# Optimization experiments

Measured on AMD Instinct MI355X. Metric: run time of the kernel, lower is better.

## Reference

```python
import jax, jax.numpy as jnp
import numpy as np

B, N = 128, 65536
POS_FRAC = 0.02  # sparse positives, realistic for detection


def setup_inputs() -> dict:
    key = jax.random.key(0)
    k1, k2 = jax.random.split(key)
    pred = jax.random.normal(k1, (B, N), dtype=jnp.float32)
    label = (jax.random.uniform(k2, (B, N)) < POS_FRAC).astype(jnp.float32)
    return {"pred": pred, "label": label}


def _focal_loss_with_mask(pred, label, gamma=2.0, alpha=0.75, negative_ratio=3.0):
    # BCE with logits, elementwise: y*softplus(-x) + (1-y)*softplus(x)
    loss = label * jax.nn.softplus(-pred) + (1.0 - label) * jax.nn.softplus(pred)
    p = jax.nn.sigmoid(pred)
    p_t = label * p + (1.0 - label) * (1.0 - p)
    loss = loss * (1.0 - p_t) ** gamma
    loss = loss * (label * alpha + (1.0 - label) * (1.0 - alpha))

    fn_mask = (p < 0.5) & (label == 1.0)
    fp_mask = (p >= 0.5) & (label == 0.0)

    # --- hard negative mining (vectorized rank-based selection) ---
    pos_mask = label > 0
    num_pos = pos_mask.sum(axis=1, keepdims=True)              # [B,1]
    num_neg = jnp.floor(negative_ratio * num_pos).astype(jnp.int32)  # int() truncation as in torch
    loss_m = jnp.where(pos_mask, -jnp.inf, loss)               # positives sorted last
    order = jnp.argsort(-loss_m, axis=1)                       # descending sort indices
    ranks = jnp.argsort(order, axis=1)                         # rank of each element
    neg_mask = ranks < num_neg
    relevant = pos_mask | neg_mask

    w = alpha / (1.0 - alpha)
    loss = jnp.where(fn_mask | fp_mask, loss * w, loss)
    rm = relevant.astype(loss.dtype)
    return (loss * rm).sum() / rm.sum()


def reference(pred, label):
    return _focal_loss_with_mask(pred, label)
```

## Files before the change

### kernel.cpp

```cpp
#include <hip/hip_runtime.h>
#include <cstdint>
#include <cstddef>

constexpr int B_ROWS = 128;
constexpr int N_COLS = 65536;
constexpr int CAP    = 4096;

constexpr size_t OFF_SLABCNT = 0;
constexpr size_t OFF_SLABNP  = (size_t)8 << 20;
constexpr size_t OFF_SLABSP  = ((size_t)8 << 20) + 4096;
constexpr size_t OFF_CAND    = (size_t)9 << 20;
constexpr size_t OFF_MISC    = (size_t)12 << 20;
constexpr size_t MO_NUMPOS   = 0;
constexpr size_t MO_SPOS     = 512;
constexpr size_t MO_CANDBIN  = 1024;
constexpr size_t MO_R1       = 1536;
constexpr size_t MO_KARR     = 2048;
constexpr size_t MO_CANDCNT  = 2560;
constexpr size_t MO_SABOVE   = 3072;
constexpr size_t MO_AUTO64   = 3584;
constexpr size_t MO_GNUM     = 4608;
constexpr size_t MO_GDEN     = 4616;
constexpr size_t MO_GDONE    = 4620;
constexpr size_t OFF_KEYS    = (size_t)16 << 20;

__device__ __forceinline__ unsigned key_from_pred(float x) {
  unsigned b = __float_as_uint(x);
  return (b & 0x80000000u) ? ~b : (b | 0x80000000u);
}
__device__ __forceinline__ float pred_from_key(unsigned k) {
  unsigned b = (k & 0x80000000u) ? (k ^ 0x80000000u) : ~k;
  return __uint_as_float(b);
}

__device__ __forceinline__ float neg_loss(float x) {
  float ax = fabsf(x);
  float e  = expf(-ax);
  float p  = (x >= 0.0f) ? 1.0f / (1.0f + e) : e / (1.0f + e);
  float sp = fmaxf(x, 0.0f) + log1pf(e);
  float f  = p;
  float l  = sp * f * f * 0.25f;
  return (p >= 0.5f) ? l * 3.0f : l;
}
__device__ __forceinline__ float pos_loss(float x) {
  float ax = fabsf(x);
  float e  = expf(-ax);
  float p  = (x >= 0.0f) ? 1.0f / (1.0f + e) : e / (1.0f + e);
  float sp = fmaxf(-x, 0.0f) + log1pf(e);
  float f  = 1.0f - p;
  float l  = sp * f * f * 0.75f;
  return (p < 0.5f) ? l * 3.0f : l;
}
__device__ __forceinline__ float loss_from_key(unsigned k) { return neg_loss(pred_from_key(k)); }

__device__ void suffix_scan(int* c, float* l, int M) {
  const int T = blockDim.x;
  const int i0 = threadIdx.x, i1 = threadIdx.x + T;
  for (int d = 1; d < M; d <<= 1) {
    int vi0 = 0, vi1 = 0; float vf0 = 0.0f, vf1 = 0.0f;
    const bool h0 = i0 < M, h1 = i1 < M;
    if (h0) { vi0 = c[i0] + ((i0 + d < M) ? c[i0 + d] : 0);
              vf0 = l[i0] + ((i0 + d < M) ? l[i0 + d] : 0.0f); }
    if (h1) { vi1 = c[i1] + ((i1 + d < M) ? c[i1 + d] : 0);
              vf1 = l[i1] + ((i1 + d < M) ? l[i1 + d] : 0.0f); }
    __syncthreads();
    if (h0) { c[i0] = vi0; l[i0] = vf0; }
    if (h1) { c[i1] = vi1; l[i1] = vf1; }
    __syncthreads();
  }
}
__device__ void suffix_scan_i(int* c, int M) {
  const int T = blockDim.x;
  const int i0 = threadIdx.x, i1 = threadIdx.x + T;
  for (int d = 1; d < M; d <<= 1) {
    int v0 = 0, v1 = 0;
    const bool h0 = i0 < M, h1 = i1 < M;
    if (h0) v0 = c[i0] + ((i0 + d < M) ? c[i0 + d] : 0);
    if (h1) v1 = c[i1] + ((i1 + d < M) ? c[i1 + d] : 0);
    __syncthreads();
    if (h0) c[i0] = v0;
    if (h1) c[i1] = v1;
    __syncthreads();
  }
}
__device__ int find_cut(const int* sc, int M, int r, int* ctrl) {
  __syncthreads();
  if (threadIdx.x == 0) *ctrl = -1;
  __syncthreads();
  int loc = -1;
  for (int i = threadIdx.x; i < M; i += blockDim.x)
    if (sc[i] >= r) loc = i;
  if (loc >= 0) atomicMax(ctrl, loc);
  __syncthreads();
  return *ctrl;
}

constexpr int K1_TPB = 256;
constexpr int K1_SEGS = 8;
constexpr int K1_SEG_ELEMS = N_COLS / K1_SEGS;
constexpr int K1_ITERS = K1_SEG_ELEMS / (K1_TPB * 4);

template <bool STORE_KEYS>
__global__ __launch_bounds__(K1_TPB)
void k1_hist(const float* __restrict__ pred, const float* __restrict__ label,
             int* __restrict__ slabCnt, int* __restrict__ slabNP, float* __restrict__ slabSP,
             unsigned* __restrict__ keys)
{
  __shared__ int   hcnt[2048];
  __shared__ int   wnp[K1_TPB / 64];
  __shared__ float wsp[K1_TPB / 64];
  const int tid = threadIdx.x;
  for (int i = tid; i < 2048; i += K1_TPB) hcnt[i] = 0;
  __syncthreads();

  const int blk = blockIdx.x;
  const size_t base = (size_t)blk * K1_SEG_ELEMS;
  const float4* p4 = reinterpret_cast<const float4*>(pred + base);
  const float4* l4 = reinterpret_cast<const float4*>(label + base);
  uint4* k4 = STORE_KEYS ? reinterpret_cast<uint4*>(keys + base) : nullptr;

  int npos = 0; float spos = 0.0f;
  for (int it = 0; it < K1_ITERS; ++it) {
    const int vi = it * K1_TPB + tid;
    const float4 pv = p4[vi];
    const float4 lv = l4[vi];
    const float xs[4] = {pv.x, pv.y, pv.z, pv.w};
    const float ys[4] = {lv.x, lv.y, lv.z, lv.w};
    unsigned ks[4];
#pragma unroll
    for (int j = 0; j < 4; ++j) {
      const float x = xs[j];
      if (ys[j] > 0.5f) {
        npos += 1;
        spos += pos_loss(x);
        ks[j] = 0u;
      } else {
        const unsigned key = key_from_pred(x);
        ks[j] = key;
        atomicAdd(&hcnt[key >> 21], 1);
      }
    }
    if (STORE_KEYS) { uint4 uk; uk.x = ks[0]; uk.y = ks[1]; uk.z = ks[2]; uk.w = ks[3]; k4[vi] = uk; }
  }

#pragma unroll
  for (int off = 32; off > 0; off >>= 1) {
    npos += __shfl_down(npos, off);
    spos += __shfl_down(spos, off);
  }
  const int wid = tid >> 6, lane = tid & 63;
  if (lane == 0) { wnp[wid] = npos; wsp[wid] = spos; }
  __syncthreads();
  if (tid == 0) {
    int tn = 0; float ts = 0.0f;
    for (int i = 0; i < K1_TPB / 64; ++i) { tn += wnp[i]; ts += wsp[i]; }
    slabNP[blk] = tn;
    slabSP[blk] = ts;
  }
  for (int i = tid; i < 2048; i += K1_TPB)
    slabCnt[(size_t)blk * 2048 + i] = hcnt[i];
}

__global__ __launch_bounds__(1024)
void k2a_cut(const int* __restrict__ slabCnt, const int* __restrict__ slabNP,
             const float* __restrict__ slabSP,
             int* __restrict__ numPos, float* __restrict__ SPos,
             int* __restrict__ candBin, unsigned long long* __restrict__ auto64,
             int* __restrict__ r1Arr, int* __restrict__ kArr,
             int* __restrict__ candCnt, float* __restrict__ S_above,
             double* __restrict__ gNum, int* __restrict__ gDen, int* __restrict__ gDone)
{
  __shared__ int s_cnt[2048];
  __shared__ int s_ctrl;
  __shared__ int s_np;
  __shared__ float s_sp;
  const int tid = threadIdx.x, row = blockIdx.x;

  if (tid == 0) {
    int tn = 0; float ts = 0.0f;
    for (int s = 0; s < K1_SEGS; ++s) { tn += slabNP[row * K1_SEGS + s]; ts += slabSP[row * K1_SEGS + s]; }
    s_np = tn; s_sp = ts;
  }
  for (int i = tid; i < 2048; i += 1024) {
    int v = 0;
#pragma unroll
    for (int s = 0; s < K1_SEGS; ++s) v += slabCnt[((size_t)(row * K1_SEGS + s)) * 2048 + i];
    s_cnt[i] = v;
  }
  __syncthreads();

  const int np = s_np;
  const int nneg = N_COLS - np;
  const int k = (3 * np < nneg) ? 3 * np : nneg;

  suffix_scan_i(s_cnt, 2048);
  int b1 = -1;
  if (k > 0) b1 = find_cut(s_cnt, 2048, k, &s_ctrl);

  if (tid == 0) {
    numPos[row]  = np;
    SPos[row]    = s_sp;
    candCnt[row] = 0;
    S_above[row] = 0.0f;
    kArr[row]    = k;
    if (k > 0) {
      const int above = (b1 + 1 < 2048) ? s_cnt[b1 + 1] : 0;
      candBin[row] = b1;
      auto64[row]  = (unsigned long long)(b1 + 1) << 21;
      r1Arr[row]   = k - above;
    } else {
      candBin[row] = -1;
      auto64[row]  = 1ull << 32;
      r1Arr[row]   = 0;
    }
  }
  if (row == 0 && tid == 1) { *gNum = 0.0; *gDen = 0; *gDone = 0; }
}

constexpr int K2B_TPB = 256;
constexpr int K2B_SEGS = 16;
constexpr int K2B_SEG_ELEMS = N_COLS / K2B_SEGS;
constexpr int K2B_ITERS = K2B_SEG_ELEMS / (K2B_TPB * 4);

template <bool USE_KEYS>
__global__ __launch_bounds__(K2B_TPB)
void k2b_stream(const float* __restrict__ pred, const float* __restrict__ label,
                const unsigned* __restrict__ keys,
                const int* __restrict__ candBin, const unsigned long long* __restrict__ auto64,
                unsigned* __restrict__ candList, int* __restrict__ candCnt,
                float* __restrict__ S_above)
{
  __shared__ unsigned s_cand[K2B_SEG_ELEMS];
  __shared__ int      s_cnt;
  __shared__ int      s_base;
  __shared__ float    wacc[K2B_TPB / 64];

  const int tid = threadIdx.x;
  const int row = blockIdx.x / K2B_SEGS;
  const int seg = blockIdx.x % K2B_SEGS;
  const size_t base = (size_t)row * N_COLS + (size_t)seg * K2B_SEG_ELEMS;
  const int cb = candBin[row];
  const unsigned long long at = auto64[row];
  const int lane = tid & 63, wid = tid >> 6;

  if (tid == 0) s_cnt = 0;
  __syncthreads();

  float acc = 0.0f;
  for (int it = 0; it < K2B_ITERS; ++it) {
    unsigned ks[4];
    if (USE_KEYS) {
      const uint4 kv = reinterpret_cast<const uint4*>(keys + base)[it * K2B_TPB + tid];
      ks[0] = kv.x; ks[1] = kv.y; ks[2] = kv.z; ks[3] = kv.w;
    } else {
      const float4 pv = reinterpret_cast<const float4*>(pred + base)[it * K2B_TPB + tid];
      const float4 lv = reinterpret_cast<const float4*>(label + base)[it * K2B_TPB + tid];
      const float xs[4] = {pv.x, pv.y, pv.z, pv.w};
      const float ys[4] = {lv.x, lv.y, lv.z, lv.w};
#pragma unroll
      for (int j = 0; j < 4; ++j) ks[j] = (ys[j] > 0.5f) ? 0u : key_from_pred(xs[j]);
    }
#pragma unroll
    for (int j = 0; j < 4; ++j) {
      const unsigned key = ks[j];
      if (key == 0u) continue;
      if ((unsigned long long)key >= at) {
        acc += loss_from_key(key);
      } else if ((int)(key >> 21) == cb) {
        const int idx = atomicAdd(&s_cnt, 1);
        s_cand[idx] = key;
      }
    }
  }

#pragma unroll
  for (int off = 32; off > 0; off >>= 1) acc += __shfl_down(acc, off);
  if (lane == 0) wacc[wid] = acc;
  __syncthreads();
  if (tid == 0) {
    float t = 0.0f;
    for (int i = 0; i < K2B_TPB / 64; ++i) t += wacc[i];
    unsafeAtomicAdd(&S_above[row], t);
    s_base = atomicAdd(&candCnt[row], s_cnt);
  }
  __syncthreads();

  const int cnt = s_cnt, gbase = s_base;
  for (int i = tid; i < cnt; i += K2B_TPB) {
    const int g = gbase + i;
    if (g < CAP) candList[(size_t)row * CAP + g] = s_cand[i];
  }
}

template <bool USE_KEYS>
__device__ void stream_bin(const float* __restrict__ pred, const float* __restrict__ label,
                           const unsigned* __restrict__ keys, int row, int b1, int b2,
                           int* hcnt, float* hloss)
{
  const size_t base = (size_t)row * N_COLS;
  const int tid = threadIdx.x;
  for (int it = 0; it < N_COLS / (1024 * 4); ++it) {
    unsigned ks[4];
    if (USE_KEYS) {
      const uint4 kv = reinterpret_cast<const uint4*>(keys + base)[it * 1024 + tid];
      ks[0] = kv.x; ks[1] = kv.y; ks[2] = kv.z; ks[3] = kv.w;
    } else {
      const float4 pv = reinterpret_cast<const float4*>(pred + base)[it * 1024 + tid];
      const float4 lv = reinterpret_cast<const float4*>(label + base)[it * 1024 + tid];
      const float xs[4] = {pv.x, pv.y, pv.z, pv.w};
      const float ys[4] = {lv.x, lv.y, lv.z, lv.w};
#pragma unroll
      for (int j = 0; j < 4; ++j) ks[j] = (ys[j] > 0.5f) ? 0u : key_from_pred(xs[j]);
    }
#pragma unroll
    for (int j = 0; j < 4; ++j) {
      const unsigned key = ks[j];
      if (!key) continue;
      if ((int)(key >> 21) != b1) continue;
      if (b2 < 0) {
        const int b = (key >> 10) & 0x7FF;
        atomicAdd(&hcnt[b], 1);
        atomicAdd(&hloss[b], loss_from_key(key));
      } else {
        if ((int)((key >> 10) & 0x7FF) != b2) continue;
        const int b = key & 0x3FF;
        atomicAdd(&hcnt[b], 1);
        atomicAdd(&hloss[b], loss_from_key(key));
      }
    }
  }
}

template <bool USE_KEYS>
__global__ __launch_bounds__(1024)
void k2c_refine(const float* __restrict__ pred, const float* __restrict__ label,
                const unsigned* __restrict__ keys,
                const int* __restrict__ numPos, const float* __restrict__ SPos,
                const int* __restrict__ candBin, const int* __restrict__ r1Arr,
                const int* __restrict__ kArr, const int* __restrict__ candCnt,
                const unsigned* __restrict__ candList, const float* __restrict__ S_above,
                double* __restrict__ gNum, int* __restrict__ gDen, int* __restrict__ gDone,
                float* __restrict__ out)
{
  __shared__ unsigned s_key[CAP];
  __shared__ float    s_lv[CAP];
  __shared__ int      h_cnt[2048];
  __shared__ float    h_loss[2048];
  __shared__ int      r3cnt[1024];
  __shared__ float    r3loss[1024];
  __shared__ int      s_ctrl;

  const int tid = threadIdx.x, row = blockIdx.x;
  const int np = numPos[row];
  const int k  = kArr[row];
  float S = 0.0f;

  if (k > 0) {
    const int r1 = r1Arr[row];
    const int b1 = candBin[row];
    const int cc = candCnt[row];

    for (int i = tid; i < 2048; i += 1024) { h_cnt[i] = 0; h_loss[i] = 0.0f; }
    __syncthreads();

    int b2, r2;
    if (cc <= CAP) {
      for (int i = tid; i < cc; i += 1024) {
        const unsigned key = candList[(size_t)row * CAP + i];
        const float l = loss_from_key(key);
        s_key[i] = key; s_lv[i] = l;
        const int b = (key >> 10) & 0x7FF;
        atomicAdd(&h_cnt[b], 1);
        atomicAdd(&h_loss[b], l);
      }
      __syncthreads();
      suffix_scan(h_cnt, h_loss, 2048);
      b2 = find_cut(h_cnt, 2048, r1, &s_ctrl);
      r2 = r1 - ((b2 + 1 < 2048) ? h_cnt[b2 + 1] : 0);
      S += (b2 + 1 < 2048) ? h_loss[b2 + 1] : 0.0f;
      __syncthreads();

      for (int i = tid; i < 1024; i += 1024) { r3cnt[i] = 0; r3loss[i] = 0.0f; }
      __syncthreads();
      for (int i = tid; i < cc; i += 1024) {
        const unsigned key = s_key[i];
        if ((int)((key >> 10) & 0x7FF) == b2) {
          atomicAdd(&r3cnt[key & 0x3FF], 1);
          atomicAdd(&r3loss[key & 0x3FF], s_lv[i]);
        }
      }
      __syncthreads();
    } else {
      stream_bin<USE_KEYS>(pred, label, keys, row, b1, -1, h_cnt, h_loss);
      __syncthreads();
      suffix_scan(h_cnt, h_loss, 2048);
      b2 = find_cut(h_cnt, 2048, r1, &s_ctrl);
      r2 = r1 - ((b2 + 1 < 2048) ? h_cnt[b2 + 1] : 0);
      S += (b2 + 1 < 2048) ? h_loss[b2 + 1] : 0.0f;
      __syncthreads();
      for (int i = tid; i < 1024; i += 1024) { r3cnt[i] = 0; r3loss[i] = 0.0f; }
      __syncthreads();
      stream_bin<USE_KEYS>(pred, label, keys, row, b1, b2, r3cnt, r3loss);
      __syncthreads();
    }

    for (int i = tid; i < 1024; i += 1024) { h_cnt[i] = r3cnt[i]; h_loss[i] = r3loss[i]; }
    __syncthreads();
    suffix_scan(h_cnt, h_loss, 1024);
    const int b3 = find_cut(h_cnt, 1024, r2, &s_ctrl);
    const int r3 = r2 - ((b3 + 1 < 1024) ? h_cnt[b3 + 1] : 0);
    S += (b3 + 1 < 1024) ? h_loss[b3 + 1] : 0.0f;
    S += (float)r3 * (r3loss[b3] / (float)r3cnt[b3]);
  }

  if (tid == 0) {
    const double contrib = (double)SPos[row] +
                           (k > 0 ? (double)S + (double)S_above[row] : 0.0);
    const int dcontrib = np + (k > 0 ? k : 0);
    unsafeAtomicAdd(gNum, contrib);
    atomicAdd(gDen, dcontrib);
    __threadfence();
    const int old = atomicAdd(gDone, 1);
    if (old == B_ROWS - 1) {
      const double num = unsafeAtomicAdd(gNum, 0.0);
      const int    den = atomicAdd(gDen, 0);
      out[0] = (float)(num / (double)den);
    }
  }
}

extern "C" void kernel_launch(void* const* d_in, const int* in_sizes, int n_in,
                              void* d_out, int out_size, void* d_ws, size_t ws_size,
                              hipStream_t stream)
{
  const float* pred  = (const float*)d_in[0];
  const float* label = (const float*)d_in[1];
  float* out = (float*)d_out;
  char* ws = (char*)d_ws;

  int*      slabCnt = (int*)(ws + OFF_SLABCNT);
  int*      slabNP  = (int*)(ws + OFF_SLABNP);
  float*    slabSP  = (float*)(ws + OFF_SLABSP);
  unsigned* cand    = (unsigned*)(ws + OFF_CAND);
  char*     misc    = ws + OFF_MISC;
  int*      numPos  = (int*)(misc + MO_NUMPOS);
  float*    SPos    = (float*)(misc + MO_SPOS);
  int*      candBin = (int*)(misc + MO_CANDBIN);
  int*      r1Arr   = (int*)(misc + MO_R1);
  int*      kArr    = (int*)(misc + MO_KARR);
  int*      candCnt = (int*)(misc + MO_CANDCNT);
  float*    S_above = (float*)(misc + MO_SABOVE);
  unsigned long long* auto64 = (unsigned long long*)(misc + MO_AUTO64);
  double*   gNum    = (double*)(misc + MO_GNUM);
  int*      gDen    = (int*)(misc + MO_GDEN);
  int*      gDone   = (int*)(misc + MO_GDONE);
  unsigned* keys    = (unsigned*)(ws + OFF_KEYS);

  const bool useKeys = ws_size >= OFF_KEYS + (size_t)B_ROWS * N_COLS * sizeof(unsigned);

  const dim3 g1(B_ROWS * K1_SEGS), t1(K1_TPB);
  const dim3 g2a(B_ROWS), t2a(1024);
  const dim3 g2b(B_ROWS * K2B_SEGS), t2b(K2B_TPB);
  const dim3 g2c(B_ROWS), t2c(1024);

  if (useKeys) {
    k1_hist<true><<<g1, t1, 0, stream>>>(pred, label, slabCnt, slabNP, slabSP, keys);
    k2a_cut<<<g2a, t2a, 0, stream>>>(slabCnt, slabNP, slabSP, numPos, SPos, candBin, auto64,
                                     r1Arr, kArr, candCnt, S_above, gNum, gDen, gDone);
    k2b_stream<true><<<g2b, t2b, 0, stream>>>(pred, label, keys, candBin, auto64, cand, candCnt, S_above);
    k2c_refine<true><<<g2c, t2c, 0, stream>>>(pred, label, keys, numPos, SPos, candBin, r1Arr, kArr,
                                              candCnt, cand, S_above, gNum, gDen, gDone, out);
  } else {
    k1_hist<false><<<g1, t1, 0, stream>>>(pred, label, slabCnt, slabNP, slabSP, nullptr);
    k2a_cut<<<g2a, t2a, 0, stream>>>(slabCnt, slabNP, slabSP, numPos, SPos, candBin, auto64,
                                     r1Arr, kArr, candCnt, S_above, gNum, gDen, gDone);
    k2b_stream<false><<<g2b, t2b, 0, stream>>>(pred, label, nullptr, candBin, auto64, cand, candCnt, S_above);
    k2c_refine<false><<<g2c, t2c, 0, stream>>>(pred, label, nullptr, numPos, SPos, candBin, r1Arr, kArr,
                                               candCnt, cand, S_above, gNum, gDen, gDone, out);
  }
}
```

Baseline: 175.9 us.

## Fuse four-kernel pipeline into one cooperative kernel with grid syncs

Replaces the four separate launches (histogram, cut, stream, refine) with a single cooperative kernel that uses grid.sync between phases. It also drops the precomputed keys buffer, so pred and label are re-read instead. The refine phase moves from 1024-thread blocks to 256-thread blocks with a two-level suffix scan. The aim is to cut launch overhead and inter-kernel gaps, at the cost of grid-wide barriers, fewer threads per row in the refine phase, and limited grid size (four blocks per CU assumed).

After: 603.3 us. 3.43x slower.

```diff
diff --git a/kernel.cpp b/kernel.cpp
--- a/kernel.cpp
+++ b/kernel.cpp
@@ -1,10 +1,19 @@
 #include <hip/hip_runtime.h>
+#include <hip/hip_cooperative_groups.h>
 #include <cstdint>
 #include <cstddef>
+
+namespace cg = cooperative_groups;
 
 constexpr int B_ROWS = 128;
 constexpr int N_COLS = 65536;
 constexpr int CAP    = 4096;
+constexpr int TPB    = 256;
+constexpr int VB1    = 1024;
+constexpr int SEGS   = VB1 / B_ROWS;
+constexpr int SEG_ELEMS = N_COLS / SEGS;
+constexpr int ITERS  = SEG_ELEMS / (TPB * 4);
+constexpr int CAND_SH = 4096;
 
 constexpr size_t OFF_SLABCNT = 0;
 constexpr size_t OFF_SLABNP  = (size_t)8 << 20;
@@ -21,8 +30,6 @@
 constexpr size_t MO_AUTO64   = 3584;
 constexpr size_t MO_GNUM     = 4608;
 constexpr size_t MO_GDEN     = 4616;
-constexpr size_t MO_GDONE    = 4620;
-constexpr size_t OFF_KEYS    = (size_t)16 << 20;
 
 __device__ __forceinline__ unsigned key_from_pred(float x) {
   unsigned b = __float_as_uint(x);
@@ -53,36 +60,29 @@
 }
 __device__ __forceinline__ float loss_from_key(unsigned k) { return neg_loss(pred_from_key(k)); }
 
-__device__ void suffix_scan(int* c, float* l, int M) {
-  const int T = blockDim.x;
-  const int i0 = threadIdx.x, i1 = threadIdx.x + T;
-  for (int d = 1; d < M; d <<= 1) {
-    int vi0 = 0, vi1 = 0; float vf0 = 0.0f, vf1 = 0.0f;
-    const bool h0 = i0 < M, h1 = i1 < M;
-    if (h0) { vi0 = c[i0] + ((i0 + d < M) ? c[i0 + d] : 0);
-              vf0 = l[i0] + ((i0 + d < M) ? l[i0 + d] : 0.0f); }
-    if (h1) { vi1 = c[i1] + ((i1 + d < M) ? c[i1 + d] : 0);
-              vf1 = l[i1] + ((i1 + d < M) ? l[i1 + d] : 0.0f); }
-    __syncthreads();
-    if (h0) { c[i0] = vi0; l[i0] = vf0; }
-    if (h1) { c[i1] = vi1; l[i1] = vf1; }
-    __syncthreads();
-  }
-}
-__device__ void suffix_scan_i(int* c, int M) {
-  const int T = blockDim.x;
-  const int i0 = threadIdx.x, i1 = threadIdx.x + T;
-  for (int d = 1; d < M; d <<= 1) {
-    int v0 = 0, v1 = 0;
-    const bool h0 = i0 < M, h1 = i1 < M;
-    if (h0) v0 = c[i0] + ((i0 + d < M) ? c[i0 + d] : 0);
-    if (h1) v1 = c[i1] + ((i1 + d < M) ? c[i1 + d] : 0);
-    __syncthreads();
-    if (h0) c[i0] = v0;
-    if (h1) c[i1] = v1;
-    __syncthreads();
-  }
-}
+__device__ void suffix_scan_2l(int* c, float* l, int M, int* tmpc, float* tmpl) {
+  const int t = threadIdx.x;
+  const int CH = M / TPB;
+  int cs = 0; float ls = 0.0f;
+  for (int j = 0; j < CH; ++j) { cs += c[t * CH + j]; ls += l[t * CH + j]; }
+  tmpc[t] = cs; tmpl[t] = ls;
+  __syncthreads();
+  for (int d = 1; d < TPB; d <<= 1) {
+    int v = tmpc[t] + ((t + d < TPB) ? tmpc[t + d] : 0);
+    float w = tmpl[t] + ((t + d < TPB) ? tmpl[t + d] : 0.0f);
+    __syncthreads();
+    tmpc[t] = v; tmpl[t] = w;
+    __syncthreads();
+  }
+  int runc = (t + 1 < TPB) ? tmpc[t + 1] : 0;
+  float runl = (t + 1 < TPB) ? tmpl[t + 1] : 0.0f;
+  for (int j = CH - 1; j >= 0; --j) {
+    runc += c[t * CH + j]; runl += l[t * CH + j];
+    c[t * CH + j] = runc;  l[t * CH + j] = runl;
+  }
+  __syncthreads();
+}
+
 __device__ int find_cut(const int* sc, int M, int r, int* ctrl) {
   __syncthreads();
   if (threadIdx.x == 0) *ctrl = -1;
@@ -95,337 +95,237 @@
   return *ctrl;
 }
 
-constexpr int K1_TPB = 256;
-constexpr int K1_SEGS = 8;
-constexpr int K1_SEG_ELEMS = N_COLS / K1_SEGS;
-constexpr int K1_ITERS = K1_SEG_ELEMS / (K1_TPB * 4);
-
-template <bool STORE_KEYS>
-__global__ __launch_bounds__(K1_TPB)
-void k1_hist(const float* __restrict__ pred, const float* __restrict__ label,
-             int* __restrict__ slabCnt, int* __restrict__ slabNP, float* __restrict__ slabSP,
-             unsigned* __restrict__ keys)
-{
-  __shared__ int   hcnt[2048];
-  __shared__ int   wnp[K1_TPB / 64];
-  __shared__ float wsp[K1_TPB / 64];
-  const int tid = threadIdx.x;
-  for (int i = tid; i < 2048; i += K1_TPB) hcnt[i] = 0;
-  __syncthreads();
-
-  const int blk = blockIdx.x;
-  const size_t base = (size_t)blk * K1_SEG_ELEMS;
+__device__ void stream_row_bin(const float* __restrict__ pred, const float* __restrict__ label,
+                               int row, int b1, int b2, int* hcnt, float* hloss) {
+  const size_t base = (size_t)row * N_COLS;
   const float4* p4 = reinterpret_cast<const float4*>(pred + base);
   const float4* l4 = reinterpret_cast<const float4*>(label + base);
-  uint4* k4 = STORE_KEYS ? reinterpret_cast<uint4*>(keys + base) : nullptr;
-
-  int npos = 0; float spos = 0.0f;
-  for (int it = 0; it < K1_ITERS; ++it) {
-    const int vi = it * K1_TPB + tid;
-    const float4 pv = p4[vi];
-    const float4 lv = l4[vi];
+  for (int it = 0; it < N_COLS / (TPB * 4); ++it) {
+    const float4 pv = p4[it * TPB + threadIdx.x];
+    const float4 lv = l4[it * TPB + threadIdx.x];
     const float xs[4] = {pv.x, pv.y, pv.z, pv.w};
     const float ys[4] = {lv.x, lv.y, lv.z, lv.w};
-    unsigned ks[4];
 #pragma unroll
     for (int j = 0; j < 4; ++j) {
-      const float x = xs[j];
-      if (ys[j] > 0.5f) {
-        npos += 1;
-        spos += pos_loss(x);
-        ks[j] = 0u;
+      if (ys[j] > 0.5f) continue;
+      const unsigned key = key_from_pred(xs[j]);
+      if ((int)(key >> 21) != b1) continue;
+      if (b2 < 0) {
+        atomicAdd(&hcnt[(key >> 10) & 0x7FF], 1);
+        atomicAdd(&hloss[(key >> 10) & 0x7FF], neg_loss(xs[j]));
       } else {
-        const unsigned key = key_from_pred(x);
-        ks[j] = key;
-        atomicAdd(&hcnt[key >> 21], 1);
-      }
-    }
-    if (STORE_KEYS) { uint4 uk; uk.x = ks[0]; uk.y = ks[1]; uk.z = ks[2]; uk.w = ks[3]; k4[vi] = uk; }
-  }
-
-#pragma unroll
-  for (int off = 32; off > 0; off >>= 1) {
-    npos += __shfl_down(npos, off);
-    spos += __shfl_down(spos, off);
-  }
-  const int wid = tid >> 6, lane = tid & 63;
-  if (lane == 0) { wnp[wid] = npos; wsp[wid] = spos; }
-  __syncthreads();
-  if (tid == 0) {
-    int tn = 0; float ts = 0.0f;
-    for (int i = 0; i < K1_TPB / 64; ++i) { tn += wnp[i]; ts += wsp[i]; }
-    slabNP[blk] = tn;
-    slabSP[blk] = ts;
-  }
-  for (int i = tid; i < 2048; i += K1_TPB)
-    slabCnt[(size_t)blk * 2048 + i] = hcnt[i];
-}
-
-__global__ __launch_bounds__(1024)
-void k2a_cut(const int* __restrict__ slabCnt, const int* __restrict__ slabNP,
-             const float* __restrict__ slabSP,
-             int* __restrict__ numPos, float* __restrict__ SPos,
-             int* __restrict__ candBin, unsigned long long* __restrict__ auto64,
-             int* __restrict__ r1Arr, int* __restrict__ kArr,
-             int* __restrict__ candCnt, float* __restrict__ S_above,
-             double* __restrict__ gNum, int* __restrict__ gDen, int* __restrict__ gDone)
+        if ((int)((key >> 10) & 0x7FF) != b2) continue;
+        atomicAdd(&hcnt[key & 0x3FF], 1);
+        atomicAdd(&hloss[key & 0x3FF], neg_loss(xs[j]));
+      }
+    }
+  }
+}
+
+__global__ __launch_bounds__(TPB, 4)
+void fused_all(const float* __restrict__ pred, const float* __restrict__ label,
+               int* __restrict__ slabCnt, int* __restrict__ slabNP, float* __restrict__ slabSP,
+               int* __restrict__ numPos, float* __restrict__ SPosArr,
+               int* __restrict__ candBin, unsigned long long* __restrict__ auto64,
+               int* __restrict__ r1Arr, int* __restrict__ kArr,
+               int* __restrict__ candCnt, float* __restrict__ S_above,
+               unsigned* __restrict__ candList,
+               double* __restrict__ gNum, int* __restrict__ gDen,
+               float* __restrict__ out)
 {
-  __shared__ int s_cnt[2048];
-  __shared__ int s_ctrl;
-  __shared__ int s_np;
-  __shared__ float s_sp;
-  const int tid = threadIdx.x, row = blockIdx.x;
-
-  if (tid == 0) {
-    int tn = 0; float ts = 0.0f;
-    for (int s = 0; s < K1_SEGS; ++s) { tn += slabNP[row * K1_SEGS + s]; ts += slabSP[row * K1_SEGS + s]; }
-    s_np = tn; s_sp = ts;
-  }
-  for (int i = tid; i < 2048; i += 1024) {
-    int v = 0;
-#pragma unroll
-    for (int s = 0; s < K1_SEGS; ++s) v += slabCnt[((size_t)(row * K1_SEGS + s)) * 2048 + i];
-    s_cnt[i] = v;
-  }
-  __syncthreads();
-
-  const int np = s_np;
-  const int nneg = N_COLS - np;
-  const int k = (3 * np < nneg) ? 3 * np : nneg;
-
-  suffix_scan_i(s_cnt, 2048);
-  int b1 = -1;
-  if (k > 0) b1 = find_cut(s_cnt, 2048, k, &s_ctrl);
-
-  if (tid == 0) {
-    numPos[row]  = np;
-    SPos[row]    = s_sp;
-    candCnt[row] = 0;
-    S_above[row] = 0.0f;
-    kArr[row]    = k;
-    if (k > 0) {
-      const int above = (b1 + 1 < 2048) ? s_cnt[b1 + 1] : 0;
-      candBin[row] = b1;
-      auto64[row]  = (unsigned long long)(b1 + 1) << 21;
-      r1Arr[row]   = k - above;
-    } else {
-      candBin[row] = -1;
-      auto64[row]  = 1ull << 32;
-      r1Arr[row]   = 0;
-    }
-  }
-  if (row == 0 && tid == 1) { *gNum = 0.0; *gDen = 0; *gDone = 0; }
-}
-
-constexpr int K2B_TPB = 256;
-constexpr int K2B_SEGS = 16;
-constexpr int K2B_SEG_ELEMS = N_COLS / K2B_SEGS;
-constexpr int K2B_ITERS = K2B_SEG_ELEMS / (K2B_TPB * 4);
-
-template <bool USE_KEYS>
-__global__ __launch_bounds__(K2B_TPB)
-void k2b_stream(const float* __restrict__ pred, const float* __restrict__ label,
-                const unsigned* __restrict__ keys,
-                const int* __restrict__ candBin, const unsigned long long* __restrict__ auto64,
-                unsigned* __restrict__ candList, int* __restrict__ candCnt,
-                float* __restrict__ S_above)
-{
-  __shared__ unsigned s_cand[K2B_SEG_ELEMS];
-  __shared__ int      s_cnt;
-  __shared__ int      s_base;
-  __shared__ float    wacc[K2B_TPB / 64];
+  cg::grid_group grid = cg::this_grid();
+  __shared__ __align__(16) char smem[26624];
+  int*      h_cnt  = (int*)smem;
+  float*    h_loss = (float*)(smem + 8192);
+  int*      r3c    = (int*)(smem + 16384);
+  float*    r3l    = (float*)(smem + 20480);
+  int*      tmpc   = (int*)(smem + 24576);
+  float*    tmpl   = (float*)(smem + 25600);
+  unsigned* candSh = (unsigned*)smem;
+  __shared__ int   s_ctrl, s_bcast, s_base;
+  __shared__ int   wnp[TPB / 64];
+  __shared__ float wsp[TPB / 64];
 
   const int tid = threadIdx.x;
-  const int row = blockIdx.x / K2B_SEGS;
-  const int seg = blockIdx.x % K2B_SEGS;
-  const size_t base = (size_t)row * N_COLS + (size_t)seg * K2B_SEG_ELEMS;
-  const int cb = candBin[row];
-  const unsigned long long at = auto64[row];
   const int lane = tid & 63, wid = tid >> 6;
 
-  if (tid == 0) s_cnt = 0;
-  __syncthreads();
-
-  float acc = 0.0f;
-  for (int it = 0; it < K2B_ITERS; ++it) {
-    unsigned ks[4];
-    if (USE_KEYS) {
-      const uint4 kv = reinterpret_cast<const uint4*>(keys + base)[it * K2B_TPB + tid];
-      ks[0] = kv.x; ks[1] = kv.y; ks[2] = kv.z; ks[3] = kv.w;
-    } else {
-      const float4 pv = reinterpret_cast<const float4*>(pred + base)[it * K2B_TPB + tid];
-      const float4 lv = reinterpret_cast<const float4*>(label + base)[it * K2B_TPB + tid];
+  for (int vb = blockIdx.x; vb < VB1; vb += gridDim.x) {
+    for (int i = tid; i < 2048; i += TPB) h_cnt[i] = 0;
+    __syncthreads();
+    const size_t base = (size_t)vb * SEG_ELEMS;
+    const float4* p4 = reinterpret_cast<const float4*>(pred + base);
+    const float4* l4 = reinterpret_cast<const float4*>(label + base);
+    int npos = 0; float spos = 0.0f;
+    for (int it = 0; it < ITERS; ++it) {
+      const float4 pv = p4[it * TPB + tid];
+      const float4 lv = l4[it * TPB + tid];
       const float xs[4] = {pv.x, pv.y, pv.z, pv.w};
       const float ys[4] = {lv.x, lv.y, lv.z, lv.w};
 #pragma unroll
-      for (int j = 0; j < 4; ++j) ks[j] = (ys[j] > 0.5f) ? 0u : key_from_pred(xs[j]);
-    }
-#pragma unroll
-    for (int j = 0; j < 4; ++j) {
-      const unsigned key = ks[j];
-      if (key == 0u) continue;
-      if ((unsigned long long)key >= at) {
-        acc += loss_from_key(key);
-      } else if ((int)(key >> 21) == cb) {
-        const int idx = atomicAdd(&s_cnt, 1);
-        s_cand[idx] = key;
-      }
-    }
-  }
-
-#pragma unroll
-  for (int off = 32; off > 0; off >>= 1) acc += __shfl_down(acc, off);
-  if (lane == 0) wacc[wid] = acc;
-  __syncthreads();
-  if (tid == 0) {
-    float t = 0.0f;
-    for (int i = 0; i < K2B_TPB / 64; ++i) t += wacc[i];
-    unsafeAtomicAdd(&S_above[row], t);
-    s_base = atomicAdd(&candCnt[row], s_cnt);
-  }
-  __syncthreads();
-
-  const int cnt = s_cnt, gbase = s_base;
-  for (int i = tid; i < cnt; i += K2B_TPB) {
-    const int g = gbase + i;
-    if (g < CAP) candList[(size_t)row * CAP + g] = s_cand[i];
-  }
-}
-
-template <bool USE_KEYS>
-__device__ void stream_bin(const float* __restrict__ pred, const float* __restrict__ label,
-                           const unsigned* __restrict__ keys, int row, int b1, int b2,
-                           int* hcnt, float* hloss)
-{
-  const size_t base = (size_t)row * N_COLS;
-  const int tid = threadIdx.x;
-  for (int it = 0; it < N_COLS / (1024 * 4); ++it) {
-    unsigned ks[4];
-    if (USE_KEYS) {
-      const uint4 kv = reinterpret_cast<const uint4*>(keys + base)[it * 1024 + tid];
-      ks[0] = kv.x; ks[1] = kv.y; ks[2] = kv.z; ks[3] = kv.w;
-    } else {
-      const float4 pv = reinterpret_cast<const float4*>(pred + base)[it * 1024 + tid];
-      const float4 lv = reinterpret_cast<const float4*>(label + base)[it * 1024 + tid];
+      for (int j = 0; j < 4; ++j) {
+        if (ys[j] > 0.5f) { npos += 1; spos += pos_loss(xs[j]); }
+        else atomicAdd(&h_cnt[key_from_pred(xs[j]) >> 21], 1);
+      }
+    }
+#pragma unroll
+    for (int off = 32; off > 0; off >>= 1) {
+      npos += __shfl_down(npos, off);
+      spos += __shfl_down(spos, off);
+    }
+    if (lane == 0) { wnp[wid] = npos; wsp[wid] = spos; }
+    __syncthreads();
+    if (tid == 0) {
+      int tn = 0; float ts = 0.0f;
+      for (int i = 0; i < TPB / 64; ++i) { tn += wnp[i]; ts += wsp[i]; }
+      slabNP[vb] = tn; slabSP[vb] = ts;
+    }
+    for (int i = tid; i < 2048; i += TPB) slabCnt[(size_t)vb * 2048 + i] = h_cnt[i];
+    __syncthreads();
+  }
+  grid.sync();
+
+  for (int row = blockIdx.x; row < B_ROWS; row += gridDim.x) {
+    for (int i = tid; i < 2048; i += TPB) {
+      int v = 0;
+#pragma unroll
+      for (int s = 0; s < SEGS; ++s) v += slabCnt[(size_t)(row * SEGS + s) * 2048 + i];
+      h_cnt[i] = v; h_loss[i] = 0.0f;
+    }
+    if (tid == 0) {
+      int tn = 0; float ts = 0.0f;
+      for (int s = 0; s < SEGS; ++s) { tn += slabNP[row * SEGS + s]; ts += slabSP[row * SEGS + s]; }
+      s_bcast = tn; wsp[0] = ts;
+    }
+    __syncthreads();
+    const int np = s_bcast;
+    const float sp = wsp[0];
+    const int nneg = N_COLS - np;
+    const int k = (3 * np < nneg) ? 3 * np : nneg;
+    suffix_scan_2l(h_cnt, h_loss, 2048, tmpc, tmpl);
+    int b1 = -1, r1 = 0; unsigned long long at = 1ull << 32;
+    if (k > 0) {
+      b1 = find_cut(h_cnt, 2048, k, &s_ctrl);
+      const int above = (b1 + 1 < 2048) ? h_cnt[b1 + 1] : 0;
+      r1 = k - above;
+      at = (unsigned long long)(b1 + 1) << 21;
+    }
+    if (tid == 0) {
+      numPos[row] = np; SPosArr[row] = sp;
+      candBin[row] = b1; auto64[row] = at; r1Arr[row] = r1; kArr[row] = k;
+      candCnt[row] = 0; S_above[row] = 0.0f;
+    }
+    __syncthreads();
+  }
+  if (blockIdx.x == 0 && tid == 0) { *gNum = 0.0; *gDen = 0; }
+  grid.sync();
+
+  for (int vb = blockIdx.x; vb < VB1; vb += gridDim.x) {
+    const int row = vb / SEGS;
+    const int cb = candBin[row];
+    const unsigned long long at = auto64[row];
+    if (tid == 0) s_bcast = 0;
+    __syncthreads();
+    const size_t base = (size_t)vb * SEG_ELEMS;
+    const float4* p4 = reinterpret_cast<const float4*>(pred + base);
+    const float4* l4 = reinterpret_cast<const float4*>(label + base);
+    float acc = 0.0f;
+    for (int it = 0; it < ITERS; ++it) {
+      const float4 pv = p4[it * TPB + tid];
+      const float4 lv = l4[it * TPB + tid];
       const float xs[4] = {pv.x, pv.y, pv.z, pv.w};
       const float ys[4] = {lv.x, lv.y, lv.z, lv.w};
 #pragma unroll
-      for (int j = 0; j < 4; ++j) ks[j] = (ys[j] > 0.5f) ? 0u : key_from_pred(xs[j]);
-    }
-#pragma unroll
-    for (int j = 0; j < 4; ++j) {
-      const unsigned key = ks[j];
-      if (!key) continue;
-      if ((int)(key >> 21) != b1) continue;
-      if (b2 < 0) {
-        const int b = (key >> 10) & 0x7FF;
-        atomicAdd(&hcnt[b], 1);
-        atomicAdd(&hloss[b], loss_from_key(key));
+      for (int j = 0; j < 4; ++j) {
+        if (ys[j] > 0.5f) continue;
+        const unsigned key = key_from_pred(xs[j]);
+        if ((unsigned long long)key >= at) {
+          acc += neg_loss(xs[j]);
+        } else if ((int)(key >> 21) == cb) {
+          const int idx = atomicAdd(&s_bcast, 1);
+          if (idx < CAND_SH) candSh[idx] = key;
+        }
+      }
+    }
+#pragma unroll
+    for (int off = 32; off > 0; off >>= 1) acc += __shfl_down(acc, off);
+    if (lane == 0) wsp[wid] = acc;
+    __syncthreads();
+    if (tid == 0) {
+      float t = 0.0f;
+      for (int i = 0; i < TPB / 64; ++i) t += wsp[i];
+      unsafeAtomicAdd(&S_above[row], t);
+      s_base = atomicAdd(&candCnt[row], s_bcast);
+    }
+    __syncthreads();
+    const int cnt = (s_bcast < CAND_SH) ? s_bcast : CAND_SH;
+    const int gb = s_base;
+    for (int i = tid; i < cnt; i += TPB) {
+      const int g = gb + i;
+      if (g < CAP) candList[(size_t)row * CAP + g] = candSh[i];
+    }
+    __syncthreads();
+  }
+  grid.sync();
+
+  for (int row = blockIdx.x; row < B_ROWS; row += gridDim.x) {
+    const int k = kArr[row];
+    float S = 0.0f;
+    if (k > 0) {
+      const int r1 = r1Arr[row], b1 = candBin[row], cc = candCnt[row];
+      for (int i = tid; i < 2048; i += TPB) { h_cnt[i] = 0; h_loss[i] = 0.0f; }
+      __syncthreads();
+      if (cc <= CAP) {
+        for (int i = tid; i < cc; i += TPB) {
+          const unsigned key = candList[(size_t)row * CAP + i];
+          const float l = loss_from_key(key);
+          atomicAdd(&h_cnt[(key >> 10) & 0x7FF], 1);
+          atomicAdd(&h_loss[(key >> 10) & 0x7FF], l);
+        }
       } else {
-        if ((int)((key >> 10) & 0x7FF) != b2) continue;
-        const int b = key & 0x3FF;
-        atomicAdd(&hcnt[b], 1);
-        atomicAdd(&hloss[b], loss_from_key(key));
-      }
-    }
-  }
-}
-
-template <bool USE_KEYS>
-__global__ __launch_bounds__(1024)
-void k2c_refine(const float* __restrict__ pred, const float* __restrict__ label,
-                const unsigned* __restrict__ keys,
-                const int* __restrict__ numPos, const float* __restrict__ SPos,
-                const int* __restrict__ candBin, const int* __restrict__ r1Arr,
-                const int* __restrict__ kArr, const int* __restrict__ candCnt,
-                const unsigned* __restrict__ candList, const float* __restrict__ S_above,
-                double* __restrict__ gNum, int* __restrict__ gDen, int* __restrict__ gDone,
-                float* __restrict__ out)
-{
-  __shared__ unsigned s_key[CAP];
-  __shared__ float    s_lv[CAP];
-  __shared__ int      h_cnt[2048];
-  __shared__ float    h_loss[2048];
-  __shared__ int      r3cnt[1024];
-  __shared__ float    r3loss[1024];
-  __shared__ int      s_ctrl;
-
-  const int tid = threadIdx.x, row = blockIdx.x;
-  const int np = numPos[row];
-  const int k  = kArr[row];
-  float S = 0.0f;
-
-  if (k > 0) {
-    const int r1 = r1Arr[row];
-    const int b1 = candBin[row];
-    const int cc = candCnt[row];
-
-    for (int i = tid; i < 2048; i += 1024) { h_cnt[i] = 0; h_loss[i] = 0.0f; }
-    __syncthreads();
-
-    int b2, r2;
-    if (cc <= CAP) {
-      for (int i = tid; i < cc; i += 1024) {
-        const unsigned key = candList[(size_t)row * CAP + i];
-        const float l = loss_from_key(key);
-        s_key[i] = key; s_lv[i] = l;
-        const int b = (key >> 10) & 0x7FF;
-        atomicAdd(&h_cnt[b], 1);
-        atomicAdd(&h_loss[b], l);
-      }
-      __syncthreads();
-      suffix_scan(h_cnt, h_loss, 2048);
-      b2 = find_cut(h_cnt, 2048, r1, &s_ctrl);
-      r2 = r1 - ((b2 + 1 < 2048) ? h_cnt[b2 + 1] : 0);
+        stream_row_bin(pred, label, row, b1, -1, h_cnt, h_loss);
+      }
+      __syncthreads();
+      suffix_scan_2l(h_cnt, h_loss, 2048, tmpc, tmpl);
+      const int b2 = find_cut(h_cnt, 2048, r1, &s_ctrl);
+      const int r2 = r1 - ((b2 + 1 < 2048) ? h_cnt[b2 + 1] : 0);
       S += (b2 + 1 < 2048) ? h_loss[b2 + 1] : 0.0f;
       __syncthreads();
-
-      for (int i = tid; i < 1024; i += 1024) { r3cnt[i] = 0; r3loss[i] = 0.0f; }
-      __syncthreads();
-      for (int i = tid; i < cc; i += 1024) {
-        const unsigned key = s_key[i];
-        if ((int)((key >> 10) & 0x7FF) == b2) {
-          atomicAdd(&r3cnt[key & 0x3FF], 1);
-          atomicAdd(&r3loss[key & 0x3FF], s_lv[i]);
+      for (int i = tid; i < 1024; i += TPB) { r3c[i] = 0; r3l[i] = 0.0f; }
+      __syncthreads();
+      if (cc <= CAP) {
+        for (int i = tid; i < cc; i += TPB) {
+          const unsigned key = candList[(size_t)row * CAP + i];
+          if ((int)((key >> 10) & 0x7FF) == b2) {
+            atomicAdd(&r3c[key & 0x3FF], 1);
+            atomicAdd(&r3l[key & 0x3FF], loss_from_key(key));
+          }
         }
-      }
-      __syncthreads();
-    } else {
-      stream_bin<USE_KEYS>(pred, label, keys, row, b1, -1, h_cnt, h_loss);
-      __syncthreads();
-      suffix_scan(h_cnt, h_loss, 2048);
-      b2 = find_cut(h_cnt, 2048, r1, &s_ctrl);
-      r2 = r1 - ((b2 + 1 < 2048) ? h_cnt[b2 + 1] : 0);
-      S += (b2 + 1 < 2048) ? h_loss[b2 + 1] : 0.0f;
-      __syncthreads();
-      for (int i = tid; i < 1024; i += 1024) { r3cnt[i] = 0; r3loss[i] = 0.0f; }
-      __syncthreads();
-      stream_bin<USE_KEYS>(pred, label, keys, row, b1, b2, r3cnt, r3loss);
-      __syncthreads();
-    }
-
-    for (int i = tid; i < 1024; i += 1024) { h_cnt[i] = r3cnt[i]; h_loss[i] = r3loss[i]; }
-    __syncthreads();
-    suffix_scan(h_cnt, h_loss, 1024);
-    const int b3 = find_cut(h_cnt, 1024, r2, &s_ctrl);
-    const int r3 = r2 - ((b3 + 1 < 1024) ? h_cnt[b3 + 1] : 0);
-    S += (b3 + 1 < 1024) ? h_loss[b3 + 1] : 0.0f;
-    S += (float)r3 * (r3loss[b3] / (float)r3cnt[b3]);
-  }
-
-  if (tid == 0) {
-    const double contrib = (double)SPos[row] +
-                           (k > 0 ? (double)S + (double)S_above[row] : 0.0);
-    const int dcontrib = np + (k > 0 ? k : 0);
-    unsafeAtomicAdd(gNum, contrib);
-    atomicAdd(gDen, dcontrib);
-    __threadfence();
-    const int old = atomicAdd(gDone, 1);
-    if (old == B_ROWS - 1) {
-      const double num = unsafeAtomicAdd(gNum, 0.0);
-      const int    den = atomicAdd(gDen, 0);
-      out[0] = (float)(num / (double)den);
-    }
+      } else {
+        stream_row_bin(pred, label, row, b1, b2, r3c, r3l);
+      }
+      __syncthreads();
+      for (int i = tid; i < 1024; i += TPB) { h_cnt[i] = r3c[i]; h_loss[i] = r3l[i]; }
+      __syncthreads();
+      suffix_scan_2l(h_cnt, h_loss, 1024, tmpc, tmpl);
+      const int b3 = find_cut(h_cnt, 1024, r2, &s_ctrl);
+      const int r3 = r2 - ((b3 + 1 < 1024) ? h_cnt[b3 + 1] : 0);
+      S += (b3 + 1 < 1024) ? h_loss[b3 + 1] : 0.0f;
+      S += (float)r3 * (r3l[b3] / (float)r3c[b3]);
+    }
+    if (tid == 0) {
+      const double contrib = (double)SPosArr[row] +
+                             (k > 0 ? (double)S + (double)S_above[row] : 0.0);
+      unsafeAtomicAdd(gNum, contrib);
+      atomicAdd(gDen, numPos[row] + (k > 0 ? k : 0));
+    }
+    __syncthreads();
+  }
+  grid.sync();
+
+  if (blockIdx.x == 0 && tid == 0) {
+    const double num = unsafeAtomicAdd(gNum, 0.0);
+    const int    den = atomicAdd(gDen, 0);
+    out[0] = (float)(num / (double)den);
   }
 }
 
@@ -453,29 +353,21 @@
   unsigned long long* auto64 = (unsigned long long*)(misc + MO_AUTO64);
   double*   gNum    = (double*)(misc + MO_GNUM);
   int*      gDen    = (int*)(misc + MO_GDEN);
-  int*      gDone   = (int*)(misc + MO_GDONE);
-  unsigned* keys    = (unsigned*)(ws + OFF_KEYS);
-
-  const bool useKeys = ws_size >= OFF_KEYS + (size_t)B_ROWS * N_COLS * sizeof(unsigned);
-
-  const dim3 g1(B_ROWS * K1_SEGS), t1(K1_TPB);
-  const dim3 g2a(B_ROWS), t2a(1024);
-  const dim3 g2b(B_ROWS * K2B_SEGS), t2b(K2B_TPB);
-  const dim3 g2c(B_ROWS), t2c(1024);
-
-  if (useKeys) {
-    k1_hist<true><<<g1, t1, 0, stream>>>(pred, label, slabCnt, slabNP, slabSP, keys);
-    k2a_cut<<<g2a, t2a, 0, stream>>>(slabCnt, slabNP, slabSP, numPos, SPos, candBin, auto64,
-                                     r1Arr, kArr, candCnt, S_above, gNum, gDen, gDone);
-    k2b_stream<true><<<g2b, t2b, 0, stream>>>(pred, label, keys, candBin, auto64, cand, candCnt, S_above);
-    k2c_refine<true><<<g2c, t2c, 0, stream>>>(pred, label, keys, numPos, SPos, candBin, r1Arr, kArr,
-                                              candCnt, cand, S_above, gNum, gDen, gDone, out);
-  } else {
-    k1_hist<false><<<g1, t1, 0, stream>>>(pred, label, slabCnt, slabNP, slabSP, nullptr);
-    k2a_cut<<<g2a, t2a, 0, stream>>>(slabCnt, slabNP, slabSP, numPos, SPos, candBin, auto64,
-                                     r1Arr, kArr, candCnt, S_above, gNum, gDen, gDone);
-    k2b_stream<false><<<g2b, t2b, 0, stream>>>(pred, label, nullptr, candBin, auto64, cand, candCnt, S_above);
-    k2c_refine<false><<<g2c, t2c, 0, stream>>>(pred, label, nullptr, numPos, SPos, candBin, r1Arr, kArr,
-                                               candCnt, cand, S_above, gNum, gDen, gDone, out);
-  }
-}
+
+  int maxB = 0;
+  if (hipOccupancyMaxActiveBlocksPerMultiprocessor(&maxB, fused_all, TPB, 0) != hipSuccess || maxB < 1)
+    maxB = 4;
+  long long grid_ll = (long long)maxB * 256;
+  if (grid_ll > VB1) grid_ll = VB1;
+  dim3 grid((unsigned)grid_ll), block(TPB);
+
+  void* args[] = {
+    (void*)&pred, (void*)&label,
+    (void*)&slabCnt, (void*)&slabNP, (void*)&slabSP,
+    (void*)&numPos, (void*)&SPos,
+    (void*)&candBin, (void*)&auto64, (void*)&r1Arr, (void*)&kArr,
+    (void*)&candCnt, (void*)&S_above, (void*)&cand,
+    (void*)&gNum, (void*)&gDen, (void*)&out
+  };
+  hipLaunchCooperativeKernel(reinterpret_cast<void*>(fused_all), grid, block, args, 0, stream);
+}
```
